# Optimization experiments

Measured on AMD Instinct MI355X. Metric: run time of the kernel, lower is better.

## Reference

```python
import jax, jax.numpy as jnp
import numpy as np

B, S, F, H = 256, 1024, 64, 64

def setup_inputs() -> dict:
    key = jax.random.key(0)
    ks = jax.random.split(key, 6)
    x = jax.random.normal(ks[0], (B, S, F), dtype=jnp.float32)
    # Keras LSTM params: kernel [F,4H], recurrent_kernel [H,4H], bias [4H] (gate order i,f,c,o)
    kernel = jax.random.normal(ks[1], (F, 4 * H), dtype=jnp.float32) * (1.0 / np.sqrt(F))
    rec_kernel = jax.random.normal(ks[2], (H, 4 * H), dtype=jnp.float32) * (1.0 / np.sqrt(H))
    bias = jnp.zeros((4 * H,), dtype=jnp.float32)
    dense_w = jax.random.normal(ks[3], (H, 1), dtype=jnp.float32) * (1.0 / np.sqrt(H))
    dense_b = jnp.zeros((1,), dtype=jnp.float32)
    return {"x": x, "kernel": kernel, "rec_kernel": rec_kernel, "bias": bias,
            "dense_w": dense_w, "dense_b": dense_b}

def reference(x, kernel, rec_kernel, bias, dense_w, dense_b):
    # Precompute input contribution for all timesteps: [B,S,4H]
    xz = jnp.einsum('bsf,fg->bsg', x, kernel) + bias
    xz_t = jnp.transpose(xz, (1, 0, 2))  # [S,B,4H]

    def step(carry, xz_step):
        h, c = carry
        z = xz_step + h @ rec_kernel  # [B,4H]
        zi, zf, zc, zo = jnp.split(z, 4, axis=-1)
        i = jax.nn.sigmoid(zi)
        f = jax.nn.sigmoid(zf)
        o = jax.nn.sigmoid(zo)
        c_new = f * c + i * jnp.tanh(zc)
        h_new = o * jnp.tanh(c_new)
        return (h_new, c_new), h_new

    h0 = jnp.zeros((x.shape[0], rec_kernel.shape[0]), dtype=x.dtype)
    c0 = jnp.zeros_like(h0)
    _, hs = jax.lax.scan(step, (h0, c0), xz_t)  # hs: [S,B,H]
    hs = jnp.transpose(hs, (1, 0, 2))  # [B,S,H]
    out = jax.nn.sigmoid(hs @ dense_w + dense_b)  # [B,S,1]
    return out
```

## Files before the change

### kernel.cpp

```cpp
#include <hip/hip_runtime.h>

typedef __attribute__((ext_vector_type(8))) short short8;
typedef __attribute__((ext_vector_type(4))) float f32x4;

#define SS 1024
#define NB 16
#define NBLK 32
#define HROW 72

__device__ __forceinline__ float sigmoidf_(float x) {
    return __builtin_amdgcn_rcpf(1.0f + __expf(-x));
}
__device__ __forceinline__ float tanhf_(float x) {
    return 1.0f - 2.0f * __builtin_amdgcn_rcpf(__expf(2.0f * x) + 1.0f);
}
__device__ __forceinline__ unsigned short f2bf(float f) {
    unsigned int u = __float_as_uint(f);
    u += 0x7fffu + ((u >> 16) & 1u);
    return (unsigned short)(u >> 16);
}

#define RAW_BARRIER() asm volatile("s_waitcnt lgkmcnt(0)\n\ts_barrier" ::: "memory")

__global__ __launch_bounds__(256)
void xconv(const float* __restrict__ x, short* __restrict__ xA) {
    const int gid  = blockIdx.x * 256 + threadIdx.x;
    const int half = gid & 1;
    const int q    = (gid >> 1) & 3;
    const int m    = (gid >> 3) & 15;
    const int bt   = gid >> 7;
    const int t    = bt & 1023;
    const int mb   = bt >> 10;
    const float* __restrict__ xr =
        x + (((size_t)(mb * 16 + m)) * SS + t) * 64 + half * 32 + q * 8;
    const float4 a = *(const float4*)xr;
    const float4 b = *(const float4*)(xr + 4);
    short8 o;
    o[0] = (short)f2bf(a.x); o[1] = (short)f2bf(a.y);
    o[2] = (short)f2bf(a.z); o[3] = (short)f2bf(a.w);
    o[4] = (short)f2bf(b.x); o[5] = (short)f2bf(b.y);
    o[6] = (short)f2bf(b.z); o[7] = (short)f2bf(b.w);
    ((short8*)xA)[gid] = o;
}

#define MF(A, Bv, C) __builtin_amdgcn_mfma_f32_16x16x32_bf16(A, Bv, C, 0, 0, 0)

#define LOADB(VAR, G, KC) do {                                                \
    const float* __restrict__ Wsrc = ((KC) < 2) ? rk : wk;                    \
    const int kb = (((KC) & 1) << 5) + (q << 3);                              \
    const int nn = ((G) << 6) + n0;                                           \
    short8 v;                                                                 \
    v[0] = (short)f2bf(Wsrc[(kb + 0) * 256 + nn]);                            \
    v[1] = (short)f2bf(Wsrc[(kb + 1) * 256 + nn]);                            \
    v[2] = (short)f2bf(Wsrc[(kb + 2) * 256 + nn]);                            \
    v[3] = (short)f2bf(Wsrc[(kb + 3) * 256 + nn]);                            \
    v[4] = (short)f2bf(Wsrc[(kb + 4) * 256 + nn]);                            \
    v[5] = (short)f2bf(Wsrc[(kb + 5) * 256 + nn]);                            \
    v[6] = (short)f2bf(Wsrc[(kb + 6) * 256 + nn]);                            \
    v[7] = (short)f2bf(Wsrc[(kb + 7) * 256 + nn]);                            \
    VAR = v; } while (0)

#define XIDX(T) (xb0 + ((size_t)(T) << 7))

#define REGION(T, PAR, XC0, XC1, XN0, XN1, QC0, QC1, QC2, QC3,                 \
               QN0, QN1, QN2, QN3, DO_O) do {                                  \
    const short8 ha0 = *(const short8*)&hbuf[(PAR) ^ 1][m * HROW + (q << 3)];  \
    const short8 ha1 = *(const short8*)&hbuf[(PAR) ^ 1][m * HROW + 32 + (q << 3)]; \
    { const size_t o = XIDX(((T) + 4 < SS) ? (T) + 4 : SS - 1);                \
      XC0 = xsrc[o]; XC1 = xsrc[o + 1]; }                                      \
    QN0 = MF(XN1, BX01, MF(XN0, BX00, cb0));                                   \
    QN1 = MF(XN1, BX11, MF(XN0, BX10, cb1));                                   \
    QN2 = MF(XN1, BX21, MF(XN0, BX20, cb2));                                   \
    QN3 = MF(XN1, BX31, MF(XN0, BX30, cb3));                                   \
    const f32x4 z0 = MF(ha1, BH01, MF(ha0, BH00, QC0));                        \
    const f32x4 z1 = MF(ha1, BH11, MF(ha0, BH10, QC1));                        \
    const f32x4 z2 = MF(ha1, BH21, MF(ha0, BH20, QC2));                        \
    const f32x4 z3 = MF(ha1, BH31, MF(ha0, BH30, QC3));                        \
    if (DO_O) {                                                                \
        const f32x4 zzero = {0.f, 0.f, 0.f, 0.f};                              \
        const f32x4 z4 = MF(ha1, BD1, MF(ha0, BD0, zzero));                    \
        if (m == 0 && w < 2) {                                                 \
            const float zw = (w == 0) ? z4[0] : z4[1];                         \
            out[((size_t)((bb << 3) + (q << 1) + w) << 10) + (T) - 1] =        \
                sigmoidf_(zw + db0);                                           \
        }                                                                      \
    }                                                                          \
    float h0, h1;                                                              \
    { const float ig = sigmoidf_(z0[0]), fg = sigmoidf_(z1[0]),                \
                  og = sigmoidf_(z3[0]);                                       \
      cc0 = fg * cc0 + ig * tanhf_(z2[0]); h0 = og * tanhf_(cc0); }            \
    { const float ig = sigmoidf_(z0[1]), fg = sigmoidf_(z1[1]),                \
                  og = sigmoidf_(z3[1]);                                       \
      cc1 = fg * cc1 + ig * tanhf_(z2[1]); h1 = og * tanhf_(cc1); }            \
    hbuf[PAR][((q << 2) + 0) * HROW + n0] = (short)f2bf(h0);                   \
    hbuf[PAR][((q << 2) + 1) * HROW + n0] = (short)f2bf(h1);                   \
    RAW_BARRIER();                                                             \
} while (0)

__global__ __launch_bounds__(256, 1)
void lstm_pipe(const short* __restrict__ xA, const float* __restrict__ wk,
               const float* __restrict__ rk, const float* __restrict__ bias,
               const float* __restrict__ dw, const float* __restrict__ db,
               float* __restrict__ out) {
    const int bb  = blockIdx.x;
    const int tid = threadIdx.x;
    const int l   = tid & 63;
    const int w   = tid >> 6;
    const int m   = l & 15;
    const int q   = l >> 4;
    const int n0  = (w << 4) + m;

    __shared__ short hbuf[2][16 * HROW];

    for (int i = tid; i < 2 * 16 * HROW; i += 256) ((short*)hbuf)[i] = 0;
    __syncthreads();

    short8 BH00, BH01, BH10, BH11, BH20, BH21, BH30, BH31;
    short8 BX00, BX01, BX10, BX11, BX20, BX21, BX30, BX31;
    LOADB(BH00, 0, 0); LOADB(BH01, 0, 1); LOADB(BX00, 0, 2); LOADB(BX01, 0, 3);
    LOADB(BH10, 1, 0); LOADB(BH11, 1, 1); LOADB(BX10, 1, 2); LOADB(BX11, 1, 3);
    LOADB(BH20, 2, 0); LOADB(BH21, 2, 1); LOADB(BX20, 2, 2); LOADB(BX21, 2, 3);
    LOADB(BH30, 3, 0); LOADB(BH31, 3, 1); LOADB(BX30, 3, 2); LOADB(BX31, 3, 3);

    short8 BD0, BD1;
    {
        short8 v0 = {0, 0, 0, 0, 0, 0, 0, 0}, v1 = v0;
        if (m == 0) {
#pragma unroll
            for (int i = 0; i < 8; ++i) v0[i] = (short)f2bf(dw[(q << 3) + i]);
#pragma unroll
            for (int i = 0; i < 8; ++i) v1[i] = (short)f2bf(dw[32 + (q << 3) + i]);
        }
        BD0 = v0; BD1 = v1;
    }

    const float b0 = bias[n0], b1 = bias[64 + n0];
    const float b2 = bias[128 + n0], b3 = bias[192 + n0];
    const f32x4 cb0 = {b0, b0, b0, b0};
    const f32x4 cb1 = {b1, b1, b1, b1};
    const f32x4 cb2 = {b2, b2, b2, b2};
    const f32x4 cb3 = {b3, b3, b3, b3};
    const float db0 = db[0];

    const int mb  = bb >> 1;
    const int br  = ((m >> 2) << 1) | (m & 1);
    const int l16 = ((bb & 1) << 3) | br;
    const size_t xb0 = (size_t)mb * 131072 + (size_t)(((l16 << 2) | q) << 1);

    const short8* __restrict__ xsrc = (const short8*)xA;
    short8 X00 = xsrc[XIDX(0)], X01 = xsrc[XIDX(0) + 1];
    short8 X10 = xsrc[XIDX(1)], X11 = xsrc[XIDX(1) + 1];
    short8 X20 = xsrc[XIDX(2)], X21 = xsrc[XIDX(2) + 1];
    short8 X30 = xsrc[XIDX(3)], X31 = xsrc[XIDX(3) + 1];

    f32x4 qA0 = MF(X01, BX01, MF(X00, BX00, cb0));
    f32x4 qA1 = MF(X01, BX11, MF(X00, BX10, cb1));
    f32x4 qA2 = MF(X01, BX21, MF(X00, BX20, cb2));
    f32x4 qA3 = MF(X01, BX31, MF(X00, BX30, cb3));
    f32x4 qB0, qB1, qB2, qB3;

    float cc0 = 0.f, cc1 = 0.f;

    REGION(0, 0, X00, X01, X10, X11, qA0, qA1, qA2, qA3, qB0, qB1, qB2, qB3, 0);
    REGION(1, 1, X10, X11, X20, X21, qB0, qB1, qB2, qB3, qA0, qA1, qA2, qA3, 1);
    REGION(2, 0, X20, X21, X30, X31, qA0, qA1, qA2, qA3, qB0, qB1, qB2, qB3, 1);
    REGION(3, 1, X30, X31, X00, X01, qB0, qB1, qB2, qB3, qA0, qA1, qA2, qA3, 1);
    for (int t = 4; t < SS; t += 4) {
        REGION(t,     0, X00, X01, X10, X11, qA0, qA1, qA2, qA3, qB0, qB1, qB2, qB3, 1);
        REGION(t + 1, 1, X10, X11, X20, X21, qB0, qB1, qB2, qB3, qA0, qA1, qA2, qA3, 1);
        REGION(t + 2, 0, X20, X21, X30, X31, qA0, qA1, qA2, qA3, qB0, qB1, qB2, qB3, 1);
        REGION(t + 3, 1, X30, X31, X00, X01, qB0, qB1, qB2, qB3, qA0, qA1, qA2, qA3, 1);
    }
    {
        const short8 ha0 = *(const short8*)&hbuf[1][m * HROW + (q << 3)];
        const short8 ha1 = *(const short8*)&hbuf[1][m * HROW + 32 + (q << 3)];
        const f32x4 zzero = {0.f, 0.f, 0.f, 0.f};
        const f32x4 z4 = MF(ha1, BD1, MF(ha0, BD0, zzero));
        if (m == 0 && w < 2) {
            const float zw = (w == 0) ? z4[0] : z4[1];
            out[((size_t)((bb << 3) + (q << 1) + w) << 10) + SS - 1] =
                sigmoidf_(zw + db0);
        }
    }
}

extern "C" void kernel_launch(void* const* d_in, const int* in_sizes, int n_in,
                              void* d_out, int out_size, void* d_ws, size_t ws_size,
                              hipStream_t stream) {
    const float* x    = (const float*)d_in[0];
    const float* wk   = (const float*)d_in[1];
    const float* rk   = (const float*)d_in[2];
    const float* bias = (const float*)d_in[3];
    const float* dw   = (const float*)d_in[4];
    const float* db   = (const float*)d_in[5];
    float* out = (float*)d_out;

    short* xA = (short*)d_ws;

    hipLaunchKernelGGL(xconv, dim3(NB * 1024 * 128 / 256), dim3(256), 0, stream,
                       x, xA);
    hipLaunchKernelGGL(lstm_pipe, dim3(NBLK), dim3(256), 0, stream,
                       xA, wk, rk, bias, dw, db, out);
}
```

Before: 500.6 us.

## Halve batch rows per block and double block count for recurrent LSTM

Each workgroup now handles 4 batch rows instead of 8, so twice as many blocks (64) run the 1024-step recurrence in parallel. Each lane computes one hidden element instead of two, which shortens the per-step serial chain of gate math. The dense output is computed by wave 0 only. The MFMA tiles are now half used (only 4 of 16 rows are valid), so matrix work per useful row doubles. This trades MFMA efficiency for lower per-step latency and more of the GPU kept busy.

```diff
diff --git a/kernel.cpp b/kernel.cpp
--- a/kernel.cpp
+++ b/kernel.cpp
@@ -5,7 +5,7 @@
 
 #define SS 1024
 #define NB 16
-#define NBLK 32
+#define NBLK 64
 #define HROW 72
 
 __device__ __forceinline__ float sigmoidf_(float x) {
@@ -76,24 +76,19 @@
     const f32x4 z1 = MF(ha1, BH11, MF(ha0, BH10, QC1));                        \
     const f32x4 z2 = MF(ha1, BH21, MF(ha0, BH20, QC2));                        \
     const f32x4 z3 = MF(ha1, BH31, MF(ha0, BH30, QC3));                        \
-    if (DO_O) {                                                                \
+    if ((DO_O) && w == 0) {                                                    \
         const f32x4 zzero = {0.f, 0.f, 0.f, 0.f};                              \
         const f32x4 z4 = MF(ha1, BD1, MF(ha0, BD0, zzero));                    \
-        if (m == 0 && w < 2) {                                                 \
-            const float zw = (w == 0) ? z4[0] : z4[1];                         \
-            out[((size_t)((bb << 3) + (q << 1) + w) << 10) + (T) - 1] =        \
-                sigmoidf_(zw + db0);                                           \
+        if (m == 0) {                                                          \
+            out[((size_t)((bb << 2) + q) << 10) + (T) - 1] =                   \
+                sigmoidf_(z4[0] + db0);                                        \
         }                                                                      \
     }                                                                          \
-    float h0, h1;                                                              \
     { const float ig = sigmoidf_(z0[0]), fg = sigmoidf_(z1[0]),                \
                   og = sigmoidf_(z3[0]);                                       \
-      cc0 = fg * cc0 + ig * tanhf_(z2[0]); h0 = og * tanhf_(cc0); }            \
-    { const float ig = sigmoidf_(z0[1]), fg = sigmoidf_(z1[1]),                \
-                  og = sigmoidf_(z3[1]);                                       \
-      cc1 = fg * cc1 + ig * tanhf_(z2[1]); h1 = og * tanhf_(cc1); }            \
-    hbuf[PAR][((q << 2) + 0) * HROW + n0] = (short)f2bf(h0);                   \
-    hbuf[PAR][((q << 2) + 1) * HROW + n0] = (short)f2bf(h1);                   \
+      cc0 = fg * cc0 + ig * tanhf_(z2[0]);                                     \
+      const float h0 = og * tanhf_(cc0);                                       \
+      hbuf[PAR][(q << 2) * HROW + n0] = (short)f2bf(h0); }                     \
     RAW_BARRIER();                                                             \
 } while (0)
 
@@ -142,9 +137,8 @@
     const f32x4 cb3 = {b3, b3, b3, b3};
     const float db0 = db[0];
 
-    const int mb  = bb >> 1;
-    const int br  = ((m >> 2) << 1) | (m & 1);
-    const int l16 = ((bb & 1) << 3) | br;
+    const int mb  = bb >> 2;
+    const int l16 = ((bb & 3) << 2) | (m >> 2);
     const size_t xb0 = (size_t)mb * 131072 + (size_t)(((l16 << 2) | q) << 1);
 
     const short8* __restrict__ xsrc = (const short8*)xA;
@@ -159,7 +153,7 @@
     f32x4 qA3 = MF(X01, BX31, MF(X00, BX30, cb3));
     f32x4 qB0, qB1, qB2, qB3;
 
-    float cc0 = 0.f, cc1 = 0.f;
+    float cc0 = 0.f;
 
     REGION(0, 0, X00, X01, X10, X11, qA0, qA1, qA2, qA3, qB0, qB1, qB2, qB3, 0);
     REGION(1, 1, X10, X11, X20, X21, qB0, qB1, qB2, qB3, qA0, qA1, qA2, qA3, 1);
@@ -171,15 +165,14 @@
         REGION(t + 2, 0, X20, X21, X30, X31, qA0, qA1, qA2, qA3, qB0, qB1, qB2, qB3, 1);
         REGION(t + 3, 1, X30, X31, X00, X01, qB0, qB1, qB2, qB3, qA0, qA1, qA2, qA3, 1);
     }
-    {
+    if (w == 0) {
         const short8 ha0 = *(const short8*)&hbuf[1][m * HROW + (q << 3)];
         const short8 ha1 = *(const short8*)&hbuf[1][m * HROW + 32 + (q << 3)];
         const f32x4 zzero = {0.f, 0.f, 0.f, 0.f};
         const f32x4 z4 = MF(ha1, BD1, MF(ha0, BD0, zzero));
-        if (m == 0 && w < 2) {
-            const float zw = (w == 0) ? z4[0] : z4[1];
-            out[((size_t)((bb << 3) + (q << 1) + w) << 10) + SS - 1] =
-                sigmoidf_(zw + db0);
+        if (m == 0) {
+            out[((size_t)((bb << 2) + q) << 10) + SS - 1] =
+                sigmoidf_(z4[0] + db0);
         }
     }
 }
```

After: 437.2 us. 1.14x faster.
